# Performance work log

Measured on AMD Instinct MI355X. Metric: run time of the kernel, lower is better.

The kernel has to match this reference:

```python
import jax, jax.numpy as jnp
import numpy as np

N_NODES = 50000
N_EDGES = 1600000
D = 128
NUM_GRAPHS = 64


def gcn_conv(x, src, dst, ew, W, b, n):
    # PyG GCNConv: add self-loops (weight 1), symmetric normalization,
    # message = norm * (x @ W)[src], aggregated at dst, then + bias.
    loop = jnp.arange(n)
    src2 = jnp.concatenate([src, loop])
    dst2 = jnp.concatenate([dst, loop])
    ew2 = jnp.concatenate([ew, jnp.ones((n,), dtype=x.dtype)])
    deg = jax.ops.segment_sum(ew2, dst2, num_segments=n)  # [N]
    dinv = jnp.where(deg > 0, jax.lax.rsqrt(deg), 0.0)
    norm = dinv[src2] * ew2 * dinv[dst2]                  # [E+N]
    xw = x @ W                                            # [N, out]
    msg = xw[src2] * norm[:, None]                        # [E+N, out]
    return jax.ops.segment_sum(msg, dst2, num_segments=n) + b


def setup_inputs() -> dict:
    key = jax.random.key(0)
    ks = jax.random.split(key, 10)
    x = jax.random.normal(ks[0], (N_NODES, D), dtype=jnp.float32)
    edge_index = jax.random.randint(ks[1], (2, N_EDGES), 0, N_NODES, dtype=jnp.int32)
    edge_weight = jax.random.uniform(ks[2], (N_EDGES,), dtype=jnp.float32)
    batch = jnp.sort(jax.random.randint(ks[3], (N_NODES,), 0, NUM_GRAPHS, dtype=jnp.int32))
    s = 1.0 / np.sqrt(D)
    W0 = jax.random.uniform(ks[4], (D, D), jnp.float32, -s, s)
    W1 = jax.random.uniform(ks[5], (D, D), jnp.float32, -s, s)
    W2 = jax.random.uniform(ks[6], (D, D), jnp.float32, -s, s)
    b0 = jnp.zeros((D,), jnp.float32)
    b1 = jnp.zeros((D,), jnp.float32)
    b2 = jnp.zeros((D,), jnp.float32)
    return {"x": x, "edge_index": edge_index, "edge_weight": edge_weight,
            "batch": batch, "W0": W0, "b0": b0, "W1": W1, "b1": b1,
            "W2": W2, "b2": b2}


def reference(x, edge_index, edge_weight, batch, W0, b0, W1, b1, W2, b2):
    src, dst = edge_index[0], edge_index[1]
    n = x.shape[0]
    h = gcn_conv(x, src, dst, edge_weight, W0, b0, n)
    h = jax.nn.relu(h)  # dropout=0.0 (eval)
    h = gcn_conv(h, src, dst, edge_weight, W1, b1, n)
    h = jax.nn.relu(h)
    h = gcn_conv(h, src, dst, edge_weight, W2, b2, n)
    # global mean pool over graphs in the batch
    sums = jax.ops.segment_sum(h, batch, num_segments=NUM_GRAPHS)
    cnts = jax.ops.segment_sum(jnp.ones((n,), h.dtype), batch, num_segments=NUM_GRAPHS)
    return sums / jnp.maximum(cnts, 1.0)[:, None]
```

## Files before the change

### kernel.cpp

```cpp
#include <hip/hip_runtime.h>
#include <hip/hip_fp16.h>


#define DFEAT 128
#define BLK_E 4096
#define NPART 8

typedef _Float16 half8 __attribute__((ext_vector_type(8)));
typedef float floatx4 __attribute__((ext_vector_type(4)));

__device__ __forceinline__ int wave_incl_scan(int v) {
    int incl = v;
    #pragma unroll
    for (int off = 1; off < 64; off <<= 1) {
        int u = __shfl_up(incl, (unsigned)off, 64);
        if ((int)(threadIdx.x & 63) >= off) incl += u;
    }
    return incl;
}

__device__ __forceinline__ void wconv_elem(int idx, const float* __restrict__ W0,
                                           const float* __restrict__ W1,
                                           const float* __restrict__ W2,
                                           _Float16* __restrict__ Wsw) {
    if (idx >= 3 * 128 * 128) return;
    int w = idx >> 14;
    int r = idx & 16383;
    int k = r >> 7, nn = r & 127;
    const float* W = (w == 0) ? W0 : (w == 1) ? W1 : W2;
    float v = W[k * 128 + nn];
    _Float16 hi = (_Float16)v;
    _Float16 lo = (_Float16)((v - (float)hi) * 1024.0f);
    int kk = k >> 5, quad = (k >> 3) & 3, j = k & 7;
    int t = nn >> 4, L = quad * 16 + (nn & 15);
    int off = ((kk * 8 + t) * 64 + L) * 8 + j;
    Wsw[(size_t)(w * 2 + 0) * 16384 + off] = hi;
    Wsw[(size_t)(w * 2 + 1) * 16384 + off] = lo;
}

__global__ __launch_bounds__(256) void hist_k(const int* __restrict__ dst,
                                              int* __restrict__ hist,
                                              const float* __restrict__ W0,
                                              const float* __restrict__ W1,
                                              const float* __restrict__ W2,
                                              _Float16* __restrict__ Wsw,
                                              float* __restrict__ out,
                                              int E, int nblk, int nbuck) {
    __shared__ int h[256];
    int tid = threadIdx.x, b = blockIdx.x;
    h[tid] = 0;
    if (b < 48) {
        #pragma unroll
        for (int k = 0; k < 4; k++)
            wconv_elem(b * 1024 + k * 256 + tid, W0, W1, W2, Wsw);
    }
    if (b < 8) {
        floatx4 z = {0.f, 0.f, 0.f, 0.f};
        ((floatx4*)out)[b * 256 + tid] = z;
    }
    __syncthreads();
    int base = b * BLK_E;
    int nE = min(BLK_E, E - base);
    for (int i = tid; i < nE; i += 256) atomicAdd(&h[dst[base + i] >> 8], 1);
    __syncthreads();
    if (tid < nbuck) hist[tid * nblk + b] = h[tid];
}

__global__ __launch_bounds__(256) void scanb_k(int* __restrict__ arr,
                                               int* __restrict__ blksum,
                                               const int* __restrict__ batch,
                                               int* __restrict__ gend,
                                               int n_val, int n_scan,
                                               int N, int ngraph) {
    int tid = threadIdx.x;
    int base = blockIdx.x * 2048 + tid * 8;
    int v[8], tsum = 0;
    #pragma unroll
    for (int j = 0; j < 8; j++) {
        v[j] = (base + j < n_val) ? arr[base + j] : 0;
        tsum += v[j];
    }
    int incl = wave_incl_scan(tsum);
    __shared__ int wtot[4];
    if ((tid & 63) == 63) wtot[tid >> 6] = incl;
    __syncthreads();
    int woff = 0;
    for (int w = 0; w < (tid >> 6); w++) woff += wtot[w];
    int run = woff + incl - tsum;
    #pragma unroll
    for (int j = 0; j < 8; j++) {
        if (base + j < n_scan) arr[base + j] = run;
        run += v[j];
    }
    if (tid == 255) blksum[blockIdx.x] = woff + incl;
    int stride = gridDim.x * 256;
    for (int i = blockIdx.x * 256 + tid; i < N; i += stride) {
        int b0 = batch[i];
        int b1 = (i + 1 < N) ? batch[i + 1] : ngraph;
        if (i == 0) for (int g = 0; g < b0; g++) gend[g] = 0;
        if (b0 != b1) for (int g = b0; g < b1; g++) gend[g] = i + 1;
    }
}

__global__ __launch_bounds__(1024) void scat_k(const int* __restrict__ src,
                                               const int* __restrict__ dst,
                                               const float* __restrict__ ew,
                                               const int* __restrict__ offs,
                                               const int* __restrict__ blksum,
                                               const int* __restrict__ gend,
                                               float* __restrict__ pool_inv,
                                               uint2* __restrict__ rec,
                                               int E, int nblk, int nbuck,
                                               int nsb, int ngraph) {
    __shared__ int lcur[256];
    __shared__ int gbase[256];
    __shared__ uint2 srec[BLK_E];
    __shared__ int gpos[BLK_E];
    __shared__ int wtot[4];
    __shared__ int bsc[64];
    int tid = threadIdx.x, b = blockIdx.x;
    if (tid < 256) lcur[tid] = 0;
    if (tid >= 256 && tid < 320) {
        int t = tid - 256;
        int v = (t < nsb) ? blksum[t] : 0;
        int incl = wave_incl_scan(v);
        bsc[t] = incl - v;
    }
    if (b == 0 && tid >= 320 && tid < 384) {
        int t = tid - 320;
        if (t < ngraph) {
            int c = gend[t] - (t ? gend[t - 1] : 0);
            pool_inv[t] = 1.0f / fmaxf((float)c, 1.0f);
        }
    }
    __syncthreads();
    int base = b * BLK_E;
    int nE = min(BLK_E, E - base);
    for (int i = tid; i < nE; i += 1024) atomicAdd(&lcur[dst[base + i] >> 8], 1);
    __syncthreads();
    int v = 0, incl = 0;
    if (tid < 256) { v = lcur[tid]; incl = wave_incl_scan(v); }
    if (tid < 256 && (tid & 63) == 63) wtot[tid >> 6] = incl;
    __syncthreads();
    if (tid < 256) {
        int woff = 0;
        for (int w = 0; w < (tid >> 6); w++) woff += wtot[w];
        int excl = woff + incl - v;
        lcur[tid] = excl;
        int oidx = tid * nblk + b;
        gbase[tid] = (tid < nbuck) ? (offs[oidx] + bsc[oidx >> 11] - excl) : 0;
    }
    __syncthreads();
    for (int i = tid; i < nE; i += 1024) {
        int e = base + i;
        int d = dst[e];
        int bin = d >> 8;
        int slot = atomicAdd(&lcur[bin], 1);
        uint2 r;
        r.x = (unsigned)src[e] | ((unsigned)(d & 255) << 16);
        r.y = __float_as_uint(ew[e]);
        srec[slot] = r;
        gpos[slot] = gbase[bin] + slot;
    }
    __syncthreads();
    for (int i = tid; i < nE; i += 1024) rec[gpos[i]] = srec[i];
}

__global__ __launch_bounds__(1024) void bucket_k(const uint2* __restrict__ rec,
                                                 const int* __restrict__ offs,
                                                 const int* __restrict__ blksum,
                                                 float* __restrict__ dinv,
                                                 int* __restrict__ rp8,
                                                 unsigned* __restrict__ csr,
                                                 int N, int nblk, int nsb) {
    __shared__ int cnt[2048];
    __shared__ unsigned degfx[256];
    __shared__ int cur[2048];
    __shared__ int wtot[16];
    __shared__ int bsc[64];
    int tid = threadIdx.x, bin = blockIdx.x;
    cnt[tid] = 0; cnt[tid + 1024] = 0;
    if (tid < 256) degfx[tid] = 0;
    if (tid >= 256 && tid < 320) {
        int t = tid - 256;
        int v = (t < nsb) ? blksum[t] : 0;
        int incl = wave_incl_scan(v);
        bsc[t] = incl - v;
    }
    __syncthreads();
    int idx0 = bin * nblk, idx1 = (bin + 1) * nblk;
    int start = offs[idx0] + bsc[idx0 >> 11];
    int endp  = offs[idx1] + bsc[idx1 >> 11];
    for (int i = start + tid; i < endp; i += 1024) {
        uint2 r = rec[i];
        int dl = (r.x >> 16) & 255;
        int part = (r.x & 0xffff) >> 13;
        atomicAdd(&cnt[dl * NPART + part], 1);
        atomicAdd(&degfx[dl], (unsigned)(__uint_as_float(r.y) * 1048576.0f + 0.5f));
    }
    __syncthreads();
    int v0 = cnt[tid * 2], v1 = cnt[tid * 2 + 1];
    int tsum = v0 + v1;
    int incl = wave_incl_scan(tsum);
    if ((tid & 63) == 63) wtot[tid >> 6] = incl;
    __syncthreads();
    int woff = 0;
    for (int w = 0; w < (tid >> 6); w++) woff += wtot[w];
    int texcl = woff + incl - tsum;
    cur[tid * 2] = texcl;
    cur[tid * 2 + 1] = texcl + v0;
    rp8[bin * 2048 + tid * 2] = start + texcl;
    rp8[bin * 2048 + tid * 2 + 1] = start + texcl + v0;
    __syncthreads();
    if (tid < 256) {
        int node = bin * 256 + tid;
        if (node < N) {
            float deg = (float)degfx[tid] * (1.0f / 1048576.0f) + 1.0f;
            float di = rsqrtf(deg);
            dinv[node] = di;
            degfx[tid] = __float_as_uint(di);
        }
    }
    __syncthreads();
    for (int i = start + tid; i < endp; i += 1024) {
        uint2 r = rec[i];
        int dl = (r.x >> 16) & 255;
        int s = r.x & 0xffff;
        int part = s >> 13;
        int p = start + atomicAdd(&cur[dl * NPART + part], 1);
        float di_d = __uint_as_float(degfx[dl]);
        float nm = __uint_as_float(r.y) * di_d;
        unsigned h = (unsigned)__half_as_ushort(__float2half_rn(nm));
        csr[p] = (unsigned)s | (h << 16);
    }
}

__global__ __launch_bounds__(512) void gemm_mfma(const _Float16* __restrict__ A,
                                                 const _Float16* __restrict__ Wsw,
                                                 const float* __restrict__ dinv,
                                                 _Float16* __restrict__ C, int n) {
    __shared__ _Float16 Bl[2 * 16384];
    {
        const uint4* s = (const uint4*)Wsw;
        uint4* d = (uint4*)Bl;
        for (int i = threadIdx.x; i < 4096; i += 512) d[i] = s[i];
    }
    int wave = threadIdx.x >> 6, lane = threadIdx.x & 63;
    int quad = lane >> 4, mcol = lane & 15;
    int row0 = blockIdx.x * 128 + wave * 16 + mcol;
    half8 af[4] = {};
    if (row0 < n) {
        const half8* Arow = (const half8*)(A + (size_t)row0 * DFEAT);
        af[0] = Arow[0 + quad];
        af[1] = Arow[4 + quad];
        af[2] = Arow[8 + quad];
        af[3] = Arow[12 + quad];
    }
    __syncthreads();
    floatx4 acch[8] = {};
    floatx4 accl[8] = {};
    const half8* Bh = (const half8*)Bl;
    const half8* Blo = (const half8*)(Bl + 16384);
    #pragma unroll
    for (int kk = 0; kk < 4; kk++) {
        #pragma unroll
        for (int t = 0; t < 8; t++) {
            half8 bh = Bh[(kk * 8 + t) * 64 + lane];
            acch[t] = __builtin_amdgcn_mfma_f32_16x16x32_f16(af[kk], bh, acch[t], 0, 0, 0);
            half8 bl = Blo[(kk * 8 + t) * 64 + lane];
            accl[t] = __builtin_amdgcn_mfma_f32_16x16x32_f16(af[kk], bl, accl[t], 0, 0, 0);
        }
    }
    int orow_base = blockIdx.x * 128 + wave * 16 + quad * 4;
    float dv[4];
    #pragma unroll
    for (int r = 0; r < 4; r++)
        dv[r] = (orow_base + r < n) ? dinv[orow_base + r] : 0.f;
    #pragma unroll
    for (int t = 0; t < 8; t++) {
        #pragma unroll
        for (int r = 0; r < 4; r++) {
            int orow = orow_base + r;
            if (orow < n) {
                float v = (acch[t][r] + accl[t][r] * (1.0f / 1024.0f)) * dv[r];
                C[(size_t)orow * DFEAT + t * 16 + mcol] = (_Float16)v;
            }
        }
    }
}

__global__ __launch_bounds__(512) void gemm_mfma_f32(const float* __restrict__ A,
                                                     const _Float16* __restrict__ Wsw,
                                                     const float* __restrict__ dinv,
                                                     _Float16* __restrict__ C, int n) {
    __shared__ _Float16 Bl[2 * 16384];
    {
        const uint4* s = (const uint4*)Wsw;
        uint4* d = (uint4*)Bl;
        for (int i = threadIdx.x; i < 4096; i += 512) d[i] = s[i];
    }
    int wave = threadIdx.x >> 6, lane = threadIdx.x & 63;
    int quad = lane >> 4, mcol = lane & 15;
    int row0 = blockIdx.x * 128 + wave * 16 + mcol;
    half8 af[4] = {};
    if (row0 < n) {
        const float4* Arow = (const float4*)(A + (size_t)row0 * DFEAT);
        #pragma unroll
        for (int kk = 0; kk < 4; kk++) {
            float4 f0 = Arow[kk * 8 + quad * 2];
            float4 f1 = Arow[kk * 8 + quad * 2 + 1];
            half8 a;
            a[0] = (_Float16)f0.x; a[1] = (_Float16)f0.y;
            a[2] = (_Float16)f0.z; a[3] = (_Float16)f0.w;
            a[4] = (_Float16)f1.x; a[5] = (_Float16)f1.y;
            a[6] = (_Float16)f1.z; a[7] = (_Float16)f1.w;
            af[kk] = a;
        }
    }
    __syncthreads();
    floatx4 acch[8] = {};
    floatx4 accl[8] = {};
    const half8* Bh = (const half8*)Bl;
    const half8* Blo = (const half8*)(Bl + 16384);
    #pragma unroll
    for (int kk = 0; kk < 4; kk++) {
        #pragma unroll
        for (int t = 0; t < 8; t++) {
            half8 bh = Bh[(kk * 8 + t) * 64 + lane];
            acch[t] = __builtin_amdgcn_mfma_f32_16x16x32_f16(af[kk], bh, acch[t], 0, 0, 0);
            half8 bl = Blo[(kk * 8 + t) * 64 + lane];
            accl[t] = __builtin_amdgcn_mfma_f32_16x16x32_f16(af[kk], bl, accl[t], 0, 0, 0);
        }
    }
    int orow_base = blockIdx.x * 128 + wave * 16 + quad * 4;
    float dv[4];
    #pragma unroll
    for (int r = 0; r < 4; r++)
        dv[r] = (orow_base + r < n) ? dinv[orow_base + r] : 0.f;
    #pragma unroll
    for (int t = 0; t < 8; t++) {
        #pragma unroll
        for (int r = 0; r < 4; r++) {
            int orow = orow_base + r;
            if (orow < n) {
                float v = (acch[t][r] + accl[t][r] * (1.0f / 1024.0f)) * dv[r];
                C[(size_t)orow * DFEAT + t * 16 + mcol] = (_Float16)v;
            }
        }
    }
}

__global__ __launch_bounds__(256) void agg_k(const __half2* __restrict__ xw2,
                                             const int* __restrict__ rp8,
                                             const unsigned* __restrict__ csr,
                                             const float* __restrict__ dinv,
                                             const float* __restrict__ bias,
                                             __half2* __restrict__ out, int relu, int n) {
    int node = blockIdx.x * 4 + (threadIdx.x >> 6);
    if (node >= n) return;
    int lane = threadIdx.x & 63;
    float di = dinv[node];
    float2 selfv = __half22float2(xw2[(size_t)node * 64 + lane]);
    float ax = di * selfv.x, ay = di * selfv.y;
    int e = rp8[node * NPART], end = rp8[node * NPART + NPART];
    for (; e + 16 <= end; e += 16) {
        unsigned c[16];
        #pragma unroll
        for (int j = 0; j < 16; j++) c[j] = csr[e + j];
        float2 v[16];
        #pragma unroll
        for (int j = 0; j < 16; j++)
            v[j] = __half22float2(xw2[(size_t)(c[j] & 0xffff) * 64 + lane]);
        #pragma unroll
        for (int j = 0; j < 16; j++) {
            float w = __half2float(__ushort_as_half((unsigned short)(c[j] >> 16)));
            ax = fmaf(w, v[j].x, ax); ay = fmaf(w, v[j].y, ay);
        }
    }
    for (; e + 8 <= end; e += 8) {
        unsigned c[8];
        #pragma unroll
        for (int j = 0; j < 8; j++) c[j] = csr[e + j];
        float2 v[8];
        #pragma unroll
        for (int j = 0; j < 8; j++)
            v[j] = __half22float2(xw2[(size_t)(c[j] & 0xffff) * 64 + lane]);
        #pragma unroll
        for (int j = 0; j < 8; j++) {
            float w = __half2float(__ushort_as_half((unsigned short)(c[j] >> 16)));
            ax = fmaf(w, v[j].x, ax); ay = fmaf(w, v[j].y, ay);
        }
    }
    for (; e + 4 <= end; e += 4) {
        unsigned c0 = csr[e + 0], c1 = csr[e + 1];
        unsigned c2 = csr[e + 2], c3 = csr[e + 3];
        float2 v0 = __half22float2(xw2[(size_t)(c0 & 0xffff) * 64 + lane]);
        float2 v1 = __half22float2(xw2[(size_t)(c1 & 0xffff) * 64 + lane]);
        float2 v2 = __half22float2(xw2[(size_t)(c2 & 0xffff) * 64 + lane]);
        float2 v3 = __half22float2(xw2[(size_t)(c3 & 0xffff) * 64 + lane]);
        float w0 = __half2float(__ushort_as_half((unsigned short)(c0 >> 16)));
        float w1 = __half2float(__ushort_as_half((unsigned short)(c1 >> 16)));
        float w2 = __half2float(__ushort_as_half((unsigned short)(c2 >> 16)));
        float w3 = __half2float(__ushort_as_half((unsigned short)(c3 >> 16)));
        ax = fmaf(w0, v0.x, ax); ay = fmaf(w0, v0.y, ay);
        ax = fmaf(w1, v1.x, ax); ay = fmaf(w1, v1.y, ay);
        ax = fmaf(w2, v2.x, ax); ay = fmaf(w2, v2.y, ay);
        ax = fmaf(w3, v3.x, ax); ay = fmaf(w3, v3.y, ay);
    }
    for (; e < end; e++) {
        unsigned c = csr[e];
        float w = __half2float(__ushort_as_half((unsigned short)(c >> 16)));
        float2 v = __half22float2(xw2[(size_t)(c & 0xffff) * 64 + lane]);
        ax = fmaf(w, v.x, ax); ay = fmaf(w, v.y, ay);
    }
    float2 bv = ((const float2*)bias)[lane];
    ax += bv.x; ay += bv.y;
    if (relu) { ax = fmaxf(ax, 0.f); ay = fmaxf(ay, 0.f); }
    out[(size_t)node * 64 + lane] = __floats2half2_rn(ax, ay);
}

__global__ __launch_bounds__(128) void pool_k(const __half* __restrict__ h,
                                              const int* __restrict__ batch,
                                              float* __restrict__ out,
                                              const float* __restrict__ pool_inv, int n) {
    int j = threadIdx.x;
    int start = blockIdx.x * 64;
    if (start >= n) return;
    int end = start + 64; if (end > n) end = n;
    int g = batch[start];
    float acc = 0.f;
    for (int i = start; i < end; i++) {
        int bi = batch[i];
        if (bi != g) {
            atomicAdd(&out[g * DFEAT + j], acc * pool_inv[g]);
            acc = 0.f; g = bi;
        }
        acc += __half2float(h[(size_t)i * DFEAT + j]);
    }
    atomicAdd(&out[g * DFEAT + j], acc * pool_inv[g]);
}

extern "C" void kernel_launch(void* const* d_in, const int* in_sizes, int n_in,
                              void* d_out, int out_size, void* d_ws, size_t ws_size,
                              hipStream_t stream) {
    const float* x    = (const float*)d_in[0];
    const int*  eidx  = (const int*)d_in[1];
    const float* ew   = (const float*)d_in[2];
    const int*  batch = (const int*)d_in[3];
    const float* W0 = (const float*)d_in[4];
    const float* b0 = (const float*)d_in[5];
    const float* W1 = (const float*)d_in[6];
    const float* b1 = (const float*)d_in[7];
    const float* W2 = (const float*)d_in[8];
    const float* b2 = (const float*)d_in[9];
    float* out = (float*)d_out;

    const int N = in_sizes[0] / DFEAT;
    const int E = in_sizes[2];
    const int ngraph = out_size / DFEAT;
    const int* src = eidx;
    const int* dst = eidx + E;

    const int nbuck = (N + 255) / 256;
    const int nblk  = (E + BLK_E - 1) / BLK_E;
    const int total = nbuck * nblk;
    const int n_scan = total + 1;
    const int nsb = (n_scan + 2047) / 2048;

    size_t off = 0;
    auto walloc = [&](size_t bytes) -> void* {
        void* p = (char*)d_ws + off;
        off += (bytes + 255) & ~(size_t)255;
        return p;
    };
    float*   dinv    = (float*)  walloc((size_t)N * 4);
    int*     rp8     = (int*)    walloc(((size_t)nbuck * 2048 + 8) * 4);
    int*     offs    = (int*)    walloc((size_t)n_scan * 4);
    int*     blksum  = (int*)    walloc(256 * 4);
    uint2*   rec     = (uint2*)  walloc((size_t)E * 8);
    unsigned* csr    = (unsigned*)walloc((size_t)E * 4);
    _Float16* xwH    = (_Float16*)walloc((size_t)N * DFEAT * 2);
    _Float16* hH     = (_Float16*)walloc((size_t)N * DFEAT * 2);
    _Float16* Wsw    = (_Float16*)walloc((size_t)6 * 16384 * 2);
    float*   pool_inv= (float*)  walloc(64 * 4);
    int*     gend    = (int*)    walloc(64 * 4);

    hist_k<<<nblk, 256, 0, stream>>>(dst, offs, W0, W1, W2, Wsw, out,
                                     E, nblk, nbuck);
    scanb_k<<<nsb, 256, 0, stream>>>(offs, blksum, batch, gend, total, n_scan,
                                     N, ngraph);
    scat_k<<<nblk, 1024, 0, stream>>>(src, dst, ew, offs, blksum, gend, pool_inv,
                                      rec, E, nblk, nbuck, nsb, ngraph);
    bucket_k<<<nbuck, 1024, 0, stream>>>(rec, offs, blksum, dinv, rp8, csr,
                                         N, nblk, nsb);

    int gG = (N + 127) / 128;
    int gA = (N + 3) / 4;
    gemm_mfma_f32<<<gG, 512, 0, stream>>>(x, Wsw + (size_t)0 * 32768, dinv, xwH, N);
    agg_k<<<gA, 256, 0, stream>>>((const __half2*)xwH, rp8, csr, dinv, b0,
                                  (__half2*)hH, 1, N);
    gemm_mfma<<<gG, 512, 0, stream>>>(hH, Wsw + (size_t)1 * 32768, dinv, xwH, N);
    agg_k<<<gA, 256, 0, stream>>>((const __half2*)xwH, rp8, csr, dinv, b1,
                                  (__half2*)hH, 1, N);
    gemm_mfma<<<gG, 512, 0, stream>>>(hH, Wsw + (size_t)2 * 32768, dinv, xwH, N);
    agg_k<<<gA, 256, 0, stream>>>((const __half2*)xwH, rp8, csr, dinv, b2,
                                  (__half2*)hH, 0, N);

    pool_k<<<(N + 63) / 64, 128, 0, stream>>>((const __half*)hH, batch, out,
                                              pool_inv, N);
}
```

Measured before the change: 337.7 us.

## Fuse first-layer GEMM into bucket kernel, apply source dinv inside aggregation

The first-layer x@W GEMM now runs as extra blocks of the CSR bucketing kernel, so it can overlap with graph preprocessing instead of waiting for dinv. Because dinv is not ready when those blocks run, the GEMM output is left unscaled and the first aggregation multiplies each edge weight by dinv[src] via an extra gathered load. The 4-edge unrolled tail loop is removed. The trade-off is extra per-edge dinv gathers in layer 1 and a larger shared-memory footprint for the bucketing blocks.

```diff
diff --git a/kernel.cpp b/kernel.cpp
--- a/kernel.cpp
+++ b/kernel.cpp
@@ -166,19 +166,75 @@
     for (int i = tid; i < nE; i += 1024) rec[gpos[i]] = srec[i];
 }
 
-__global__ __launch_bounds__(1024) void bucket_k(const uint2* __restrict__ rec,
-                                                 const int* __restrict__ offs,
-                                                 const int* __restrict__ blksum,
-                                                 float* __restrict__ dinv,
-                                                 int* __restrict__ rp8,
-                                                 unsigned* __restrict__ csr,
-                                                 int N, int nblk, int nsb) {
-    __shared__ int cnt[2048];
-    __shared__ unsigned degfx[256];
-    __shared__ int cur[2048];
-    __shared__ int wtot[16];
-    __shared__ int bsc[64];
-    int tid = threadIdx.x, bin = blockIdx.x;
+__global__ __launch_bounds__(1024) void bucket_gemm_k(
+        const uint2* __restrict__ rec, const int* __restrict__ offs,
+        const int* __restrict__ blksum, float* __restrict__ dinv,
+        int* __restrict__ rp8, unsigned* __restrict__ csr,
+        int N, int nblk, int nsb, int nbuck,
+        const float* __restrict__ A, const _Float16* __restrict__ Wsw,
+        _Float16* __restrict__ C) {
+    __shared__ _Float16 Bl[2 * 16384];
+    int tid = threadIdx.x;
+    if (blockIdx.x >= nbuck) {
+        int bid = blockIdx.x - nbuck;
+        {
+            const uint4* s = (const uint4*)Wsw;
+            uint4* d = (uint4*)Bl;
+            for (int i = tid; i < 4096; i += 1024) d[i] = s[i];
+        }
+        int wave = tid >> 6, lane = tid & 63;
+        int quad = lane >> 4, mcol = lane & 15;
+        int row0 = bid * 256 + wave * 16 + mcol;
+        half8 af[4] = {};
+        if (row0 < N) {
+            const float4* Arow = (const float4*)(A + (size_t)row0 * DFEAT);
+            #pragma unroll
+            for (int kk = 0; kk < 4; kk++) {
+                float4 f0 = Arow[kk * 8 + quad * 2];
+                float4 f1 = Arow[kk * 8 + quad * 2 + 1];
+                half8 a;
+                a[0] = (_Float16)f0.x; a[1] = (_Float16)f0.y;
+                a[2] = (_Float16)f0.z; a[3] = (_Float16)f0.w;
+                a[4] = (_Float16)f1.x; a[5] = (_Float16)f1.y;
+                a[6] = (_Float16)f1.z; a[7] = (_Float16)f1.w;
+                af[kk] = a;
+            }
+        }
+        __syncthreads();
+        floatx4 acch[8] = {};
+        floatx4 accl[8] = {};
+        const half8* Bh = (const half8*)Bl;
+        const half8* Blo = (const half8*)(Bl + 16384);
+        #pragma unroll
+        for (int kk = 0; kk < 4; kk++) {
+            #pragma unroll
+            for (int t = 0; t < 8; t++) {
+                half8 bh = Bh[(kk * 8 + t) * 64 + lane];
+                acch[t] = __builtin_amdgcn_mfma_f32_16x16x32_f16(af[kk], bh, acch[t], 0, 0, 0);
+                half8 bl = Blo[(kk * 8 + t) * 64 + lane];
+                accl[t] = __builtin_amdgcn_mfma_f32_16x16x32_f16(af[kk], bl, accl[t], 0, 0, 0);
+            }
+        }
+        int orow_base = bid * 256 + wave * 16 + quad * 4;
+        #pragma unroll
+        for (int t = 0; t < 8; t++) {
+            #pragma unroll
+            for (int r = 0; r < 4; r++) {
+                int orow = orow_base + r;
+                if (orow < N) {
+                    float v = acch[t][r] + accl[t][r] * (1.0f / 1024.0f);
+                    C[(size_t)orow * DFEAT + t * 16 + mcol] = (_Float16)v;
+                }
+            }
+        }
+        return;
+    }
+    int* cnt = (int*)Bl;
+    int* cur = cnt + 2048;
+    int* wtot = cur + 2048;
+    int* bsc = wtot + 16;
+    unsigned* degfx = (unsigned*)(bsc + 64);
+    int bin = blockIdx.x;
     cnt[tid] = 0; cnt[tid + 1024] = 0;
     if (tid < 256) degfx[tid] = 0;
     if (tid >= 256 && tid < 320) {
@@ -289,79 +345,20 @@
     }
 }
 
-__global__ __launch_bounds__(512) void gemm_mfma_f32(const float* __restrict__ A,
-                                                     const _Float16* __restrict__ Wsw,
-                                                     const float* __restrict__ dinv,
-                                                     _Float16* __restrict__ C, int n) {
-    __shared__ _Float16 Bl[2 * 16384];
-    {
-        const uint4* s = (const uint4*)Wsw;
-        uint4* d = (uint4*)Bl;
-        for (int i = threadIdx.x; i < 4096; i += 512) d[i] = s[i];
-    }
-    int wave = threadIdx.x >> 6, lane = threadIdx.x & 63;
-    int quad = lane >> 4, mcol = lane & 15;
-    int row0 = blockIdx.x * 128 + wave * 16 + mcol;
-    half8 af[4] = {};
-    if (row0 < n) {
-        const float4* Arow = (const float4*)(A + (size_t)row0 * DFEAT);
-        #pragma unroll
-        for (int kk = 0; kk < 4; kk++) {
-            float4 f0 = Arow[kk * 8 + quad * 2];
-            float4 f1 = Arow[kk * 8 + quad * 2 + 1];
-            half8 a;
-            a[0] = (_Float16)f0.x; a[1] = (_Float16)f0.y;
-            a[2] = (_Float16)f0.z; a[3] = (_Float16)f0.w;
-            a[4] = (_Float16)f1.x; a[5] = (_Float16)f1.y;
-            a[6] = (_Float16)f1.z; a[7] = (_Float16)f1.w;
-            af[kk] = a;
-        }
-    }
-    __syncthreads();
-    floatx4 acch[8] = {};
-    floatx4 accl[8] = {};
-    const half8* Bh = (const half8*)Bl;
-    const half8* Blo = (const half8*)(Bl + 16384);
-    #pragma unroll
-    for (int kk = 0; kk < 4; kk++) {
-        #pragma unroll
-        for (int t = 0; t < 8; t++) {
-            half8 bh = Bh[(kk * 8 + t) * 64 + lane];
-            acch[t] = __builtin_amdgcn_mfma_f32_16x16x32_f16(af[kk], bh, acch[t], 0, 0, 0);
-            half8 bl = Blo[(kk * 8 + t) * 64 + lane];
-            accl[t] = __builtin_amdgcn_mfma_f32_16x16x32_f16(af[kk], bl, accl[t], 0, 0, 0);
-        }
-    }
-    int orow_base = blockIdx.x * 128 + wave * 16 + quad * 4;
-    float dv[4];
-    #pragma unroll
-    for (int r = 0; r < 4; r++)
-        dv[r] = (orow_base + r < n) ? dinv[orow_base + r] : 0.f;
-    #pragma unroll
-    for (int t = 0; t < 8; t++) {
-        #pragma unroll
-        for (int r = 0; r < 4; r++) {
-            int orow = orow_base + r;
-            if (orow < n) {
-                float v = (acch[t][r] + accl[t][r] * (1.0f / 1024.0f)) * dv[r];
-                C[(size_t)orow * DFEAT + t * 16 + mcol] = (_Float16)v;
-            }
-        }
-    }
-}
-
 __global__ __launch_bounds__(256) void agg_k(const __half2* __restrict__ xw2,
                                              const int* __restrict__ rp8,
                                              const unsigned* __restrict__ csr,
                                              const float* __restrict__ dinv,
                                              const float* __restrict__ bias,
-                                             __half2* __restrict__ out, int relu, int n) {
+                                             __half2* __restrict__ out,
+                                             int relu, int n, int raw) {
     int node = blockIdx.x * 4 + (threadIdx.x >> 6);
     if (node >= n) return;
     int lane = threadIdx.x & 63;
     float di = dinv[node];
+    float sc = raw ? di * di : di;
     float2 selfv = __half22float2(xw2[(size_t)node * 64 + lane]);
-    float ax = di * selfv.x, ay = di * selfv.y;
+    float ax = sc * selfv.x, ay = sc * selfv.y;
     int e = rp8[node * NPART], end = rp8[node * NPART + NPART];
     for (; e + 16 <= end; e += 16) {
         unsigned c[16];
@@ -371,10 +368,15 @@
         #pragma unroll
         for (int j = 0; j < 16; j++)
             v[j] = __half22float2(xw2[(size_t)(c[j] & 0xffff) * 64 + lane]);
+        float ww[16];
         #pragma unroll
         for (int j = 0; j < 16; j++) {
-            float w = __half2float(__ushort_as_half((unsigned short)(c[j] >> 16)));
-            ax = fmaf(w, v[j].x, ax); ay = fmaf(w, v[j].y, ay);
+            ww[j] = __half2float(__ushort_as_half((unsigned short)(c[j] >> 16)));
+            if (raw) ww[j] *= dinv[c[j] & 0xffff];
+        }
+        #pragma unroll
+        for (int j = 0; j < 16; j++) {
+            ax = fmaf(ww[j], v[j].x, ax); ay = fmaf(ww[j], v[j].y, ay);
         }
     }
     for (; e + 8 <= end; e += 8) {
@@ -385,31 +387,21 @@
         #pragma unroll
         for (int j = 0; j < 8; j++)
             v[j] = __half22float2(xw2[(size_t)(c[j] & 0xffff) * 64 + lane]);
+        float ww[8];
         #pragma unroll
         for (int j = 0; j < 8; j++) {
-            float w = __half2float(__ushort_as_half((unsigned short)(c[j] >> 16)));
-            ax = fmaf(w, v[j].x, ax); ay = fmaf(w, v[j].y, ay);
-        }
-    }
-    for (; e + 4 <= end; e += 4) {
-        unsigned c0 = csr[e + 0], c1 = csr[e + 1];
-        unsigned c2 = csr[e + 2], c3 = csr[e + 3];
-        float2 v0 = __half22float2(xw2[(size_t)(c0 & 0xffff) * 64 + lane]);
-        float2 v1 = __half22float2(xw2[(size_t)(c1 & 0xffff) * 64 + lane]);
-        float2 v2 = __half22float2(xw2[(size_t)(c2 & 0xffff) * 64 + lane]);
-        float2 v3 = __half22float2(xw2[(size_t)(c3 & 0xffff) * 64 + lane]);
-        float w0 = __half2float(__ushort_as_half((unsigned short)(c0 >> 16)));
-        float w1 = __half2float(__ushort_as_half((unsigned short)(c1 >> 16)));
-        float w2 = __half2float(__ushort_as_half((unsigned short)(c2 >> 16)));
-        float w3 = __half2float(__ushort_as_half((unsigned short)(c3 >> 16)));
-        ax = fmaf(w0, v0.x, ax); ay = fmaf(w0, v0.y, ay);
-        ax = fmaf(w1, v1.x, ax); ay = fmaf(w1, v1.y, ay);
-        ax = fmaf(w2, v2.x, ax); ay = fmaf(w2, v2.y, ay);
-        ax = fmaf(w3, v3.x, ax); ay = fmaf(w3, v3.y, ay);
+            ww[j] = __half2float(__ushort_as_half((unsigned short)(c[j] >> 16)));
+            if (raw) ww[j] *= dinv[c[j] & 0xffff];
+        }
+        #pragma unroll
+        for (int j = 0; j < 8; j++) {
+            ax = fmaf(ww[j], v[j].x, ax); ay = fmaf(ww[j], v[j].y, ay);
+        }
     }
     for (; e < end; e++) {
         unsigned c = csr[e];
         float w = __half2float(__ushort_as_half((unsigned short)(c >> 16)));
+        if (raw) w *= dinv[c & 0xffff];
         float2 v = __half22float2(xw2[(size_t)(c & 0xffff) * 64 + lane]);
         ax = fmaf(w, v.x, ax); ay = fmaf(w, v.y, ay);
     }
@@ -491,20 +483,23 @@
                                      N, ngraph);
     scat_k<<<nblk, 1024, 0, stream>>>(src, dst, ew, offs, blksum, gend, pool_inv,
                                       rec, E, nblk, nbuck, nsb, ngraph);
-    bucket_k<<<nbuck, 1024, 0, stream>>>(rec, offs, blksum, dinv, rp8, csr,
-                                         N, nblk, nsb);
+    int gemmb = (N + 255) / 256;
+    bucket_gemm_k<<<nbuck + gemmb, 1024, 0, stream>>>(rec, offs, blksum, dinv,
+                                                      rp8, csr, N, nblk, nsb,
+                                                      nbuck, x,
+                                                      Wsw + (size_t)0 * 32768,
+                                                      xwH);
 
     int gG = (N + 127) / 128;
     int gA = (N + 3) / 4;
-    gemm_mfma_f32<<<gG, 512, 0, stream>>>(x, Wsw + (size_t)0 * 32768, dinv, xwH, N);
     agg_k<<<gA, 256, 0, stream>>>((const __half2*)xwH, rp8, csr, dinv, b0,
-                                  (__half2*)hH, 1, N);
+                                  (__half2*)hH, 1, N, 1);
     gemm_mfma<<<gG, 512, 0, stream>>>(hH, Wsw + (size_t)1 * 32768, dinv, xwH, N);
     agg_k<<<gA, 256, 0, stream>>>((const __half2*)xwH, rp8, csr, dinv, b1,
-                                  (__half2*)hH, 1, N);
+                                  (__half2*)hH, 1, N, 0);
     gemm_mfma<<<gG, 512, 0, stream>>>(hH, Wsw + (size_t)2 * 32768, dinv, xwH, N);
     agg_k<<<gA, 256, 0, stream>>>((const __half2*)xwH, rp8, csr, dinv, b2,
-                                  (__half2*)hH, 0, N);
+                                  (__half2*)hH, 0, N, 0);
 
     pool_k<<<(N + 63) / 64, 128, 0, stream>>>((const __half*)hH, batch, out,
                                               pool_inv, N);
```

After: 385.3 us. 14.1% more time.

## Compute degrees in scatter pass and fuse first GEMM with bucket kernel

Applied to the files above, without the earlier changes.

Degree accumulation moves from fixed-point LDS atomics in the bucket kernel to global float atomics in the scatter kernel. The bucket kernel can then compute dinv up front. That lets the first-layer fp32-input GEMM run as extra blocks in the same launch, so one kernel launch goes away and the GEMM overlaps with bucketing. This adds 1.6M global atomics spread over 50K addresses, plus a memset. Because the float atomics accumulate in nondeterministic order, the summation order changes.

```diff
diff --git a/kernel.cpp b/kernel.cpp
--- a/kernel.cpp
+++ b/kernel.cpp
@@ -109,6 +109,7 @@
                                                const int* __restrict__ blksum,
                                                const int* __restrict__ gend,
                                                float* __restrict__ pool_inv,
+                                               float* __restrict__ deg,
                                                uint2* __restrict__ rec,
                                                int E, int nblk, int nbuck,
                                                int nsb, int ngraph) {
@@ -154,11 +155,13 @@
     for (int i = tid; i < nE; i += 1024) {
         int e = base + i;
         int d = dst[e];
+        float w_e = ew[e];
+        atomicAdd(&deg[d], w_e);
         int bin = d >> 8;
         int slot = atomicAdd(&lcur[bin], 1);
         uint2 r;
         r.x = (unsigned)src[e] | ((unsigned)(d & 255) << 16);
-        r.y = __float_as_uint(ew[e]);
+        r.y = __float_as_uint(w_e);
         srec[slot] = r;
         gpos[slot] = gbase[bin] + slot;
     }
@@ -166,21 +169,86 @@
     for (int i = tid; i < nE; i += 1024) rec[gpos[i]] = srec[i];
 }
 
-__global__ __launch_bounds__(1024) void bucket_k(const uint2* __restrict__ rec,
-                                                 const int* __restrict__ offs,
-                                                 const int* __restrict__ blksum,
-                                                 float* __restrict__ dinv,
-                                                 int* __restrict__ rp8,
-                                                 unsigned* __restrict__ csr,
-                                                 int N, int nblk, int nsb) {
-    __shared__ int cnt[2048];
-    __shared__ unsigned degfx[256];
-    __shared__ int cur[2048];
-    __shared__ int wtot[16];
-    __shared__ int bsc[64];
-    int tid = threadIdx.x, bin = blockIdx.x;
+__global__ __launch_bounds__(1024) void bucket_gemm_k(
+        const uint2* __restrict__ rec, const int* __restrict__ offs,
+        const int* __restrict__ blksum, const float* __restrict__ deg,
+        float* __restrict__ dinv, int* __restrict__ rp8,
+        unsigned* __restrict__ csr, int N, int nblk, int nsb, int nbuck,
+        const float* __restrict__ A, const _Float16* __restrict__ Wsw,
+        _Float16* __restrict__ C) {
+    __shared__ _Float16 Bl[2 * 16384];
+    int tid = threadIdx.x;
+    if (blockIdx.x >= nbuck) {
+        int bid = blockIdx.x - nbuck;
+        {
+            const uint4* s = (const uint4*)Wsw;
+            uint4* d = (uint4*)Bl;
+            for (int i = tid; i < 4096; i += 1024) d[i] = s[i];
+        }
+        int wave = tid >> 6, lane = tid & 63;
+        int quad = lane >> 4, mcol = lane & 15;
+        int row0 = bid * 256 + wave * 16 + mcol;
+        half8 af[4] = {};
+        if (row0 < N) {
+            const float4* Arow = (const float4*)(A + (size_t)row0 * DFEAT);
+            #pragma unroll
+            for (int kk = 0; kk < 4; kk++) {
+                float4 f0 = Arow[kk * 8 + quad * 2];
+                float4 f1 = Arow[kk * 8 + quad * 2 + 1];
+                half8 a;
+                a[0] = (_Float16)f0.x; a[1] = (_Float16)f0.y;
+                a[2] = (_Float16)f0.z; a[3] = (_Float16)f0.w;
+                a[4] = (_Float16)f1.x; a[5] = (_Float16)f1.y;
+                a[6] = (_Float16)f1.z; a[7] = (_Float16)f1.w;
+                af[kk] = a;
+            }
+        }
+        __syncthreads();
+        floatx4 acch[8] = {};
+        floatx4 accl[8] = {};
+        const half8* Bh = (const half8*)Bl;
+        const half8* Blo = (const half8*)(Bl + 16384);
+        #pragma unroll
+        for (int kk = 0; kk < 4; kk++) {
+            #pragma unroll
+            for (int t = 0; t < 8; t++) {
+                half8 bh = Bh[(kk * 8 + t) * 64 + lane];
+                acch[t] = __builtin_amdgcn_mfma_f32_16x16x32_f16(af[kk], bh, acch[t], 0, 0, 0);
+                half8 bl = Blo[(kk * 8 + t) * 64 + lane];
+                accl[t] = __builtin_amdgcn_mfma_f32_16x16x32_f16(af[kk], bl, accl[t], 0, 0, 0);
+            }
+        }
+        int orow_base = bid * 256 + wave * 16 + quad * 4;
+        float dv[4];
+        #pragma unroll
+        for (int r = 0; r < 4; r++)
+            dv[r] = (orow_base + r < N) ? rsqrtf(deg[orow_base + r] + 1.0f) : 0.f;
+        #pragma unroll
+        for (int t = 0; t < 8; t++) {
+            #pragma unroll
+            for (int r = 0; r < 4; r++) {
+                int orow = orow_base + r;
+                if (orow < N) {
+                    float v = (acch[t][r] + accl[t][r] * (1.0f / 1024.0f)) * dv[r];
+                    C[(size_t)orow * DFEAT + t * 16 + mcol] = (_Float16)v;
+                }
+            }
+        }
+        return;
+    }
+    int* cnt = (int*)Bl;
+    int* cur = cnt + 2048;
+    int* wtot = cur + 2048;
+    int* bsc = wtot + 16;
+    float* dinvl = (float*)(bsc + 64);
+    int bin = blockIdx.x;
     cnt[tid] = 0; cnt[tid + 1024] = 0;
-    if (tid < 256) degfx[tid] = 0;
+    if (tid < 256) {
+        int node = bin * 256 + tid;
+        float di = (node < N) ? rsqrtf(deg[node] + 1.0f) : 0.f;
+        dinvl[tid] = di;
+        if (node < N) dinv[node] = di;
+    }
     if (tid >= 256 && tid < 320) {
         int t = tid - 256;
         int v = (t < nsb) ? blksum[t] : 0;
@@ -196,7 +264,6 @@
         int dl = (r.x >> 16) & 255;
         int part = (r.x & 0xffff) >> 13;
         atomicAdd(&cnt[dl * NPART + part], 1);
-        atomicAdd(&degfx[dl], (unsigned)(__uint_as_float(r.y) * 1048576.0f + 0.5f));
     }
     __syncthreads();
     int v0 = cnt[tid * 2], v1 = cnt[tid * 2 + 1];
@@ -212,24 +279,13 @@
     rp8[bin * 2048 + tid * 2] = start + texcl;
     rp8[bin * 2048 + tid * 2 + 1] = start + texcl + v0;
     __syncthreads();
-    if (tid < 256) {
-        int node = bin * 256 + tid;
-        if (node < N) {
-            float deg = (float)degfx[tid] * (1.0f / 1048576.0f) + 1.0f;
-            float di = rsqrtf(deg);
-            dinv[node] = di;
-            degfx[tid] = __float_as_uint(di);
-        }
-    }
-    __syncthreads();
     for (int i = start + tid; i < endp; i += 1024) {
         uint2 r = rec[i];
         int dl = (r.x >> 16) & 255;
         int s = r.x & 0xffff;
         int part = s >> 13;
         int p = start + atomicAdd(&cur[dl * NPART + part], 1);
-        float di_d = __uint_as_float(degfx[dl]);
-        float nm = __uint_as_float(r.y) * di_d;
+        float nm = __uint_as_float(r.y) * dinvl[dl];
         unsigned h = (unsigned)__half_as_ushort(__float2half_rn(nm));
         csr[p] = (unsigned)s | (h << 16);
     }
@@ -255,67 +311,6 @@
         af[1] = Arow[4 + quad];
         af[2] = Arow[8 + quad];
         af[3] = Arow[12 + quad];
-    }
-    __syncthreads();
-    floatx4 acch[8] = {};
-    floatx4 accl[8] = {};
-    const half8* Bh = (const half8*)Bl;
-    const half8* Blo = (const half8*)(Bl + 16384);
-    #pragma unroll
-    for (int kk = 0; kk < 4; kk++) {
-        #pragma unroll
-        for (int t = 0; t < 8; t++) {
-            half8 bh = Bh[(kk * 8 + t) * 64 + lane];
-            acch[t] = __builtin_amdgcn_mfma_f32_16x16x32_f16(af[kk], bh, acch[t], 0, 0, 0);
-            half8 bl = Blo[(kk * 8 + t) * 64 + lane];
-            accl[t] = __builtin_amdgcn_mfma_f32_16x16x32_f16(af[kk], bl, accl[t], 0, 0, 0);
-        }
-    }
-    int orow_base = blockIdx.x * 128 + wave * 16 + quad * 4;
-    float dv[4];
-    #pragma unroll
-    for (int r = 0; r < 4; r++)
-        dv[r] = (orow_base + r < n) ? dinv[orow_base + r] : 0.f;
-    #pragma unroll
-    for (int t = 0; t < 8; t++) {
-        #pragma unroll
-        for (int r = 0; r < 4; r++) {
-            int orow = orow_base + r;
-            if (orow < n) {
-                float v = (acch[t][r] + accl[t][r] * (1.0f / 1024.0f)) * dv[r];
-                C[(size_t)orow * DFEAT + t * 16 + mcol] = (_Float16)v;
-            }
-        }
-    }
-}
-
-__global__ __launch_bounds__(512) void gemm_mfma_f32(const float* __restrict__ A,
-                                                     const _Float16* __restrict__ Wsw,
-                                                     const float* __restrict__ dinv,
-                                                     _Float16* __restrict__ C, int n) {
-    __shared__ _Float16 Bl[2 * 16384];
-    {
-        const uint4* s = (const uint4*)Wsw;
-        uint4* d = (uint4*)Bl;
-        for (int i = threadIdx.x; i < 4096; i += 512) d[i] = s[i];
-    }
-    int wave = threadIdx.x >> 6, lane = threadIdx.x & 63;
-    int quad = lane >> 4, mcol = lane & 15;
-    int row0 = blockIdx.x * 128 + wave * 16 + mcol;
-    half8 af[4] = {};
-    if (row0 < n) {
-        const float4* Arow = (const float4*)(A + (size_t)row0 * DFEAT);
-        #pragma unroll
-        for (int kk = 0; kk < 4; kk++) {
-            float4 f0 = Arow[kk * 8 + quad * 2];
-            float4 f1 = Arow[kk * 8 + quad * 2 + 1];
-            half8 a;
-            a[0] = (_Float16)f0.x; a[1] = (_Float16)f0.y;
-            a[2] = (_Float16)f0.z; a[3] = (_Float16)f0.w;
-            a[4] = (_Float16)f1.x; a[5] = (_Float16)f1.y;
-            a[6] = (_Float16)f1.z; a[7] = (_Float16)f1.w;
-            af[kk] = a;
-        }
     }
     __syncthreads();
     floatx4 acch[8] = {};
@@ -474,6 +469,7 @@
         return p;
     };
     float*   dinv    = (float*)  walloc((size_t)N * 4);
+    float*   deg     = (float*)  walloc((size_t)N * 4);
     int*     rp8     = (int*)    walloc(((size_t)nbuck * 2048 + 8) * 4);
     int*     offs    = (int*)    walloc((size_t)n_scan * 4);
     int*     blksum  = (int*)    walloc(256 * 4);
@@ -485,18 +481,23 @@
     float*   pool_inv= (float*)  walloc(64 * 4);
     int*     gend    = (int*)    walloc(64 * 4);
 
+    hipMemsetAsync(deg, 0, (size_t)N * 4, stream);
+
     hist_k<<<nblk, 256, 0, stream>>>(dst, offs, W0, W1, W2, Wsw, out,
                                      E, nblk, nbuck);
     scanb_k<<<nsb, 256, 0, stream>>>(offs, blksum, batch, gend, total, n_scan,
                                      N, ngraph);
     scat_k<<<nblk, 1024, 0, stream>>>(src, dst, ew, offs, blksum, gend, pool_inv,
-                                      rec, E, nblk, nbuck, nsb, ngraph);
-    bucket_k<<<nbuck, 1024, 0, stream>>>(rec, offs, blksum, dinv, rp8, csr,
-                                         N, nblk, nsb);
+                                      deg, rec, E, nblk, nbuck, nsb, ngraph);
+    int gemmb = (N + 255) / 256;
+    bucket_gemm_k<<<nbuck + gemmb, 1024, 0, stream>>>(rec, offs, blksum, deg,
+                                                      dinv, rp8, csr, N, nblk,
+                                                      nsb, nbuck, x,
+                                                      Wsw + (size_t)0 * 32768,
+                                                      xwH);
 
     int gG = (N + 127) / 128;
     int gA = (N + 3) / 4;
-    gemm_mfma_f32<<<gG, 512, 0, stream>>>(x, Wsw + (size_t)0 * 32768, dinv, xwH, N);
     agg_k<<<gA, 256, 0, stream>>>((const __half2*)xwH, rp8, csr, dinv, b0,
                                   (__half2*)hH, 1, N);
     gemm_mfma<<<gG, 512, 0, stream>>>(hH, Wsw + (size_t)1 * 32768, dinv, xwH, N);
```

Result: slower. 419.4 us (+24.2%).
